# Kernel optimization log

Hardware: AMD Instinct MI355X
Metric: run time of the kernel (lower is better)

The kernel has to match this reference:

```python
import jax, jax.numpy as jnp
import numpy as np

NEG = -1000.0  # fill value for unmatched (type_mask != ti) entries

B, N, R = 4, 48, 16
T = 2 * R + 1          # 33 transition channels
Nc, L = 80, 3          # chains, chain length
Nt, Ni = 16, 5         # triples, chains per triple (uniform c_sections)


def setup_inputs() -> dict:
    key = jax.random.key(0)
    k1, k2, k3, k4, k5 = jax.random.split(key, 5)
    transitions = jax.random.normal(k1, (B, N, N, T), dtype=jnp.float32)
    type_mask = jax.random.randint(k2, (B, N, N, R), 0, 2, dtype=jnp.int32)
    rules = jax.random.randint(k3, (Nc, L), 0, T, dtype=jnp.int32)
    # stacked per-triple weights [Nt, Ni] (orig: ParameterList of [Ni,1]) and biases [Nt]
    weights = jax.random.normal(k4, (Nt, Ni), dtype=jnp.float32) / np.sqrt(Ni)
    biases = jax.random.uniform(k5, (Nt,), dtype=jnp.float32, minval=-1.0, maxval=1.0)
    return {"transitions": transitions, "type_mask": type_mask, "rules": rules,
            "weights": weights, "biases": biases}


def path_scores(transitions, rules):
    """Tropical (max-plus) chain DP.
    transitions: [B,N,N,T], rules: [Nc,L] -> scores [B,N,N,Nc]
    scores[b,x,y,c] = max over intermediate nodes of sum of hop scores.
    """
    Lc = rules.shape[1]
    hops = [transitions[..., rules[:, l]] for l in range(Lc)]  # each [B,N,N,Nc]
    # max-plus "matmul": s[b,x,y,c] = max_k hops0[b,x,k,c] + hops1[b,k,y,c]
    s = jnp.max(hops[0][:, :, :, None, :] + hops[1][:, None, :, :, :], axis=2)
    for l in range(2, Lc):
        s = jnp.max(s[:, :, :, None, :] + hops[l][:, None, :, :, :], axis=2)
    return s


def reference(transitions, type_mask, rules, weights, biases):
    # scores over all chains, exponentiated: [B,N,N,Nc]
    s = jnp.exp(path_scores(transitions, rules))
    # group chains by triple (uniform sections): [B,N,N,Nt,Ni]
    s = s.reshape(s.shape[0], s.shape[1], s.shape[2], Nt, Ni)
    # per-triple weighted sum + bias; one triple per relation so Nt == R
    comb = jnp.einsum('bxytc,tc->bxyt', s, weights) + biases  # [B,N,N,R]
    # masked_scatter: write score where type_mask[...,i] == ti (== 0 here), else -1000
    out = jnp.where(type_mask == 0, comb, NEG)
    return out
```

## Files before the change

kernel.cpp:

```cpp
#include <hip/hip_runtime.h>
#include <cmath>

#define BB 4
#define NN 48
#define NP 49
#define TT 33
#define RR 16
#define NC 80
#define NI 5

__global__ __launch_bounds__(192) void chain_dp_kernel(
    const float* __restrict__ trans,
    const int*   __restrict__ rules,
    const float* __restrict__ weights,
    float*       __restrict__ sw)
{
    __shared__ float H0T[NN * NP];
    __shared__ float H1 [NN * NN];
    __shared__ float H2 [NN * NN];
    __shared__ float S1T[NN * NP];

    const int bc = blockIdx.x;
    const int b  = bc / NC;
    const int c  = bc - b * NC;

    const int r0 = rules[c * 3 + 0];
    const int r1 = rules[c * 3 + 1];
    const int r2 = rules[c * 3 + 2];
    const float w = weights[c];

    const float* tb = trans + (size_t)b * NN * NN * TT;

    for (int i = threadIdx.x; i < NN * NN; i += 192) {
        const int x = i / NN;
        const int k = i - x * NN;
        const size_t base = (size_t)i * TT;
        H0T[k * NP + x] = tb[base + r0];
        H1[i]           = tb[base + r1];
        H2[i]           = tb[base + r2];
    }
    __syncthreads();

    const int tx = threadIdx.x & 15;
    const int ty = threadIdx.x >> 4;
    const int x0 = tx * 3;
    const int y0 = ty * 4;

    float acc[3][4];
    #pragma unroll
    for (int jx = 0; jx < 3; ++jx)
        #pragma unroll
        for (int jy = 0; jy < 4; ++jy) acc[jx][jy] = -INFINITY;

    #pragma unroll 4
    for (int k = 0; k < NN; ++k) {
        const float a0 = H0T[k * NP + x0 + 0];
        const float a1 = H0T[k * NP + x0 + 1];
        const float a2 = H0T[k * NP + x0 + 2];
        const float4 bv = *(const float4*)&H1[k * NN + y0];
        acc[0][0] = fmaxf(acc[0][0], a0 + bv.x);
        acc[0][1] = fmaxf(acc[0][1], a0 + bv.y);
        acc[0][2] = fmaxf(acc[0][2], a0 + bv.z);
        acc[0][3] = fmaxf(acc[0][3], a0 + bv.w);
        acc[1][0] = fmaxf(acc[1][0], a1 + bv.x);
        acc[1][1] = fmaxf(acc[1][1], a1 + bv.y);
        acc[1][2] = fmaxf(acc[1][2], a1 + bv.z);
        acc[1][3] = fmaxf(acc[1][3], a1 + bv.w);
        acc[2][0] = fmaxf(acc[2][0], a2 + bv.x);
        acc[2][1] = fmaxf(acc[2][1], a2 + bv.y);
        acc[2][2] = fmaxf(acc[2][2], a2 + bv.z);
        acc[2][3] = fmaxf(acc[2][3], a2 + bv.w);
    }

    #pragma unroll
    for (int jx = 0; jx < 3; ++jx)
        #pragma unroll
        for (int jy = 0; jy < 4; ++jy)
            S1T[(y0 + jy) * NP + x0 + jx] = acc[jx][jy];
    __syncthreads();

    float acc2[3][4];
    #pragma unroll
    for (int jx = 0; jx < 3; ++jx)
        #pragma unroll
        for (int jy = 0; jy < 4; ++jy) acc2[jx][jy] = -INFINITY;

    #pragma unroll 4
    for (int k = 0; k < NN; ++k) {
        const float a0 = S1T[k * NP + x0 + 0];
        const float a1 = S1T[k * NP + x0 + 1];
        const float a2 = S1T[k * NP + x0 + 2];
        const float4 bv = *(const float4*)&H2[k * NN + y0];
        acc2[0][0] = fmaxf(acc2[0][0], a0 + bv.x);
        acc2[0][1] = fmaxf(acc2[0][1], a0 + bv.y);
        acc2[0][2] = fmaxf(acc2[0][2], a0 + bv.z);
        acc2[0][3] = fmaxf(acc2[0][3], a0 + bv.w);
        acc2[1][0] = fmaxf(acc2[1][0], a1 + bv.x);
        acc2[1][1] = fmaxf(acc2[1][1], a1 + bv.y);
        acc2[1][2] = fmaxf(acc2[1][2], a1 + bv.z);
        acc2[1][3] = fmaxf(acc2[1][3], a1 + bv.w);
        acc2[2][0] = fmaxf(acc2[2][0], a2 + bv.x);
        acc2[2][1] = fmaxf(acc2[2][1], a2 + bv.y);
        acc2[2][2] = fmaxf(acc2[2][2], a2 + bv.z);
        acc2[2][3] = fmaxf(acc2[2][3], a2 + bv.w);
    }

    float* outp = sw + (size_t)bc * NN * NN;
    #pragma unroll
    for (int jx = 0; jx < 3; ++jx)
        #pragma unroll
        for (int jy = 0; jy < 4; ++jy)
            outp[(x0 + jx) * NN + y0 + jy] = __expf(acc2[jx][jy]) * w;
}

__global__ __launch_bounds__(256) void combine_kernel(
    const float* __restrict__ sw,
    const int*   __restrict__ mask,
    const float* __restrict__ biases,
    float*       __restrict__ out)
{
    const int idx = blockIdx.x * 256 + threadIdx.x;
    if (idx >= BB * NN * NN) return;
    const int b = idx / (NN * NN);
    const int p = idx - b * (NN * NN);

    const float* base = sw + (size_t)b * NC * NN * NN + p;

    float acc[RR];
    #pragma unroll
    for (int t = 0; t < RR; ++t) {
        float s = biases[t];
        #pragma unroll
        for (int i = 0; i < NI; ++i)
            s += base[(size_t)(t * NI + i) * NN * NN];
        acc[t] = s;
    }

    const int4* m4 = (const int4*)(mask + (size_t)idx * RR);
    float4*     o4 = (float4*)(out + (size_t)idx * RR);
    #pragma unroll
    for (int q = 0; q < 4; ++q) {
        const int4 m = m4[q];
        float4 o;
        o.x = (m.x == 0) ? acc[q * 4 + 0] : -1000.0f;
        o.y = (m.y == 0) ? acc[q * 4 + 1] : -1000.0f;
        o.z = (m.z == 0) ? acc[q * 4 + 2] : -1000.0f;
        o.w = (m.w == 0) ? acc[q * 4 + 3] : -1000.0f;
        o4[q] = o;
    }
}

extern "C" void kernel_launch(void* const* d_in, const int* in_sizes, int n_in,
                              void* d_out, int out_size, void* d_ws, size_t ws_size,
                              hipStream_t stream)
{
    const float* trans   = (const float*)d_in[0];
    const int*   mask    = (const int*)  d_in[1];
    const int*   rules   = (const int*)  d_in[2];
    const float* weights = (const float*)d_in[3];
    const float* biases  = (const float*)d_in[4];
    float* out = (float*)d_out;
    float* sw  = (float*)d_ws;

    chain_dp_kernel<<<BB * NC, 192, 0, stream>>>(trans, rules, weights, sw);

    const int total = BB * NN * NN;
    combine_kernel<<<(total + 255) / 256, 256, 0, stream>>>(sw, mask, biases, out);
}
```

Before: 75.47 us.

## Split chain DP over x-halves and k-halves, widen combine parallelism

The chain DP grid is doubled so that each block handles half of the x rows. Within a block the two thread groups each take half of the k reduction, and their partial maxima are merged through shared memory, which gives more blocks to fill the GPU. The combine kernel likewise splits the 16 relations across two threads per pixel. The cost is that every block still loads the full H1 and H2 matrices, so redundant global loads roughly double, and extra syncs and merge passes are added.

```diff
diff --git a/kernel.cpp b/kernel.cpp
--- a/kernel.cpp
+++ b/kernel.cpp
@@ -3,48 +3,61 @@
 
 #define BB 4
 #define NN 48
-#define NP 49
 #define TT 33
 #define RR 16
 #define NC 80
 #define NI 5
-
-__global__ __launch_bounds__(192) void chain_dp_kernel(
+#define NEG (-1000.0f)
+
+#define XS 24
+#define XP 25
+#define NTH 192
+#define NTILE 96
+
+__global__ __launch_bounds__(NTH) void chain_dp_kernel(
     const float* __restrict__ trans,
     const int*   __restrict__ rules,
     const float* __restrict__ weights,
     float*       __restrict__ sw)
 {
-    __shared__ float H0T[NN * NP];
+    __shared__ float H0T[NN * XP];
     __shared__ float H1 [NN * NN];
     __shared__ float H2 [NN * NN];
-    __shared__ float S1T[NN * NP];
-
-    const int bc = blockIdx.x;
-    const int b  = bc / NC;
-    const int c  = bc - b * NC;
+    __shared__ float S1T[NN * XP];
+    __shared__ float Pa [NN * XP];
+
+    const int blk = blockIdx.x;
+    const int bc  = blk >> 1;
+    const int xh  = blk & 1;
+    const int b   = bc / NC;
+    const int c   = bc - b * NC;
+    const int xbase = xh * XS;
 
     const int r0 = rules[c * 3 + 0];
     const int r1 = rules[c * 3 + 1];
     const int r2 = rules[c * 3 + 2];
-    const float w = weights[c];
 
     const float* tb = trans + (size_t)b * NN * NN * TT;
 
-    for (int i = threadIdx.x; i < NN * NN; i += 192) {
-        const int x = i / NN;
-        const int k = i - x * NN;
+    for (int i = threadIdx.x; i < XS * NN; i += NTH) {
+        const int xl = i / NN;
+        const int k  = i - xl * NN;
+        H0T[k * XP + xl] = tb[(size_t)((xbase + xl) * NN + k) * TT + r0];
+    }
+    for (int i = threadIdx.x; i < NN * NN; i += NTH) {
         const size_t base = (size_t)i * TT;
-        H0T[k * NP + x] = tb[base + r0];
-        H1[i]           = tb[base + r1];
-        H2[i]           = tb[base + r2];
-    }
-    __syncthreads();
-
-    const int tx = threadIdx.x & 15;
-    const int ty = threadIdx.x >> 4;
+        H1[i] = tb[base + r1];
+        H2[i] = tb[base + r2];
+    }
+    __syncthreads();
+
+    const int g  = threadIdx.x / NTILE;
+    const int w  = threadIdx.x - g * NTILE;
+    const int tx = w & 7;
+    const int ty = w >> 3;
     const int x0 = tx * 3;
     const int y0 = ty * 4;
+    const int k0 = g * 24;
 
     float acc[3][4];
     #pragma unroll
@@ -53,64 +66,87 @@
         for (int jy = 0; jy < 4; ++jy) acc[jx][jy] = -INFINITY;
 
     #pragma unroll 4
-    for (int k = 0; k < NN; ++k) {
-        const float a0 = H0T[k * NP + x0 + 0];
-        const float a1 = H0T[k * NP + x0 + 1];
-        const float a2 = H0T[k * NP + x0 + 2];
-        const float4 bv = *(const float4*)&H1[k * NN + y0];
-        acc[0][0] = fmaxf(acc[0][0], a0 + bv.x);
-        acc[0][1] = fmaxf(acc[0][1], a0 + bv.y);
-        acc[0][2] = fmaxf(acc[0][2], a0 + bv.z);
-        acc[0][3] = fmaxf(acc[0][3], a0 + bv.w);
-        acc[1][0] = fmaxf(acc[1][0], a1 + bv.x);
-        acc[1][1] = fmaxf(acc[1][1], a1 + bv.y);
-        acc[1][2] = fmaxf(acc[1][2], a1 + bv.z);
-        acc[1][3] = fmaxf(acc[1][3], a1 + bv.w);
-        acc[2][0] = fmaxf(acc[2][0], a2 + bv.x);
-        acc[2][1] = fmaxf(acc[2][1], a2 + bv.y);
-        acc[2][2] = fmaxf(acc[2][2], a2 + bv.z);
-        acc[2][3] = fmaxf(acc[2][3], a2 + bv.w);
-    }
-
+    for (int kp = 0; kp < 12; ++kp) {
+        const int k = k0 + kp * 2;
+        float a0[3], a1[3];
+        #pragma unroll
+        for (int jx = 0; jx < 3; ++jx) {
+            a0[jx] = H0T[k * XP + x0 + jx];
+            a1[jx] = H0T[(k + 1) * XP + x0 + jx];
+        }
+        const float4 bv0 = *(const float4*)&H1[k * NN + y0];
+        const float4 bv1 = *(const float4*)&H1[(k + 1) * NN + y0];
+        const float b0[4] = {bv0.x, bv0.y, bv0.z, bv0.w};
+        const float b1[4] = {bv1.x, bv1.y, bv1.z, bv1.w};
+        #pragma unroll
+        for (int jx = 0; jx < 3; ++jx)
+            #pragma unroll
+            for (int jy = 0; jy < 4; ++jy)
+                acc[jx][jy] = fmaxf(acc[jx][jy],
+                                    fmaxf(a0[jx] + b0[jy], a1[jx] + b1[jy]));
+    }
+
+    {
+        float* dst = (g == 0) ? S1T : Pa;
+        #pragma unroll
+        for (int jx = 0; jx < 3; ++jx)
+            #pragma unroll
+            for (int jy = 0; jy < 4; ++jy)
+                dst[(y0 + jy) * XP + x0 + jx] = acc[jx][jy];
+    }
+    __syncthreads();
+
+    for (int j = threadIdx.x; j < NN * XP; j += NTH)
+        S1T[j] = fmaxf(S1T[j], Pa[j]);
+    __syncthreads();
+
+    float acc2[3][4];
     #pragma unroll
     for (int jx = 0; jx < 3; ++jx)
         #pragma unroll
-        for (int jy = 0; jy < 4; ++jy)
-            S1T[(y0 + jy) * NP + x0 + jx] = acc[jx][jy];
-    __syncthreads();
-
-    float acc2[3][4];
-    #pragma unroll
-    for (int jx = 0; jx < 3; ++jx)
-        #pragma unroll
         for (int jy = 0; jy < 4; ++jy) acc2[jx][jy] = -INFINITY;
 
     #pragma unroll 4
-    for (int k = 0; k < NN; ++k) {
-        const float a0 = S1T[k * NP + x0 + 0];
-        const float a1 = S1T[k * NP + x0 + 1];
-        const float a2 = S1T[k * NP + x0 + 2];
-        const float4 bv = *(const float4*)&H2[k * NN + y0];
-        acc2[0][0] = fmaxf(acc2[0][0], a0 + bv.x);
-        acc2[0][1] = fmaxf(acc2[0][1], a0 + bv.y);
-        acc2[0][2] = fmaxf(acc2[0][2], a0 + bv.z);
-        acc2[0][3] = fmaxf(acc2[0][3], a0 + bv.w);
-        acc2[1][0] = fmaxf(acc2[1][0], a1 + bv.x);
-        acc2[1][1] = fmaxf(acc2[1][1], a1 + bv.y);
-        acc2[1][2] = fmaxf(acc2[1][2], a1 + bv.z);
-        acc2[1][3] = fmaxf(acc2[1][3], a1 + bv.w);
-        acc2[2][0] = fmaxf(acc2[2][0], a2 + bv.x);
-        acc2[2][1] = fmaxf(acc2[2][1], a2 + bv.y);
-        acc2[2][2] = fmaxf(acc2[2][2], a2 + bv.z);
-        acc2[2][3] = fmaxf(acc2[2][3], a2 + bv.w);
-    }
-
-    float* outp = sw + (size_t)bc * NN * NN;
-    #pragma unroll
-    for (int jx = 0; jx < 3; ++jx)
-        #pragma unroll
-        for (int jy = 0; jy < 4; ++jy)
-            outp[(x0 + jx) * NN + y0 + jy] = __expf(acc2[jx][jy]) * w;
+    for (int kp = 0; kp < 12; ++kp) {
+        const int k = k0 + kp * 2;
+        float a0[3], a1[3];
+        #pragma unroll
+        for (int jx = 0; jx < 3; ++jx) {
+            a0[jx] = S1T[k * XP + x0 + jx];
+            a1[jx] = S1T[(k + 1) * XP + x0 + jx];
+        }
+        const float4 bv0 = *(const float4*)&H2[k * NN + y0];
+        const float4 bv1 = *(const float4*)&H2[(k + 1) * NN + y0];
+        const float b0[4] = {bv0.x, bv0.y, bv0.z, bv0.w};
+        const float b1[4] = {bv1.x, bv1.y, bv1.z, bv1.w};
+        #pragma unroll
+        for (int jx = 0; jx < 3; ++jx)
+            #pragma unroll
+            for (int jy = 0; jy < 4; ++jy)
+                acc2[jx][jy] = fmaxf(acc2[jx][jy],
+                                     fmaxf(a0[jx] + b0[jy], a1[jx] + b1[jy]));
+    }
+
+    if (g == 1) {
+        #pragma unroll
+        for (int jx = 0; jx < 3; ++jx)
+            #pragma unroll
+            for (int jy = 0; jy < 4; ++jy)
+                Pa[(jx * 4 + jy) * NTILE + w] = acc2[jx][jy];
+    }
+    __syncthreads();
+
+    if (g == 0) {
+        const float wgt = weights[c];
+        float* outp = sw + (size_t)bc * NN * NN;
+        #pragma unroll
+        for (int jx = 0; jx < 3; ++jx)
+            #pragma unroll
+            for (int jy = 0; jy < 4; ++jy) {
+                const float m = fmaxf(acc2[jx][jy], Pa[(jx * 4 + jy) * NTILE + w]);
+                outp[(xbase + x0 + jx) * NN + y0 + jy] = __expf(m) * wgt;
+            }
+    }
 }
 
 __global__ __launch_bounds__(256) void combine_kernel(
@@ -119,33 +155,35 @@
     const float* __restrict__ biases,
     float*       __restrict__ out)
 {
-    const int idx = blockIdx.x * 256 + threadIdx.x;
-    if (idx >= BB * NN * NN) return;
-    const int b = idx / (NN * NN);
-    const int p = idx - b * (NN * NN);
+    const int tq = threadIdx.x >> 7;
+    const int pl = blockIdx.x * 128 + (threadIdx.x & 127);
+    if (pl >= BB * NN * NN) return;
+    const int b = pl / (NN * NN);
+    const int p = pl - b * (NN * NN);
 
     const float* base = sw + (size_t)b * NC * NN * NN + p;
 
-    float acc[RR];
-    #pragma unroll
-    for (int t = 0; t < RR; ++t) {
+    float acc[8];
+    #pragma unroll
+    for (int tt = 0; tt < 8; ++tt) {
+        const int t = tq * 8 + tt;
         float s = biases[t];
         #pragma unroll
         for (int i = 0; i < NI; ++i)
             s += base[(size_t)(t * NI + i) * NN * NN];
-        acc[t] = s;
-    }
-
-    const int4* m4 = (const int4*)(mask + (size_t)idx * RR);
-    float4*     o4 = (float4*)(out + (size_t)idx * RR);
-    #pragma unroll
-    for (int q = 0; q < 4; ++q) {
+        acc[tt] = s;
+    }
+
+    const int4* m4 = (const int4*)(mask + (size_t)pl * RR + tq * 8);
+    float4*     o4 = (float4*)(out + (size_t)pl * RR + tq * 8);
+    #pragma unroll
+    for (int q = 0; q < 2; ++q) {
         const int4 m = m4[q];
         float4 o;
-        o.x = (m.x == 0) ? acc[q * 4 + 0] : -1000.0f;
-        o.y = (m.y == 0) ? acc[q * 4 + 1] : -1000.0f;
-        o.z = (m.z == 0) ? acc[q * 4 + 2] : -1000.0f;
-        o.w = (m.w == 0) ? acc[q * 4 + 3] : -1000.0f;
+        o.x = (m.x == 0) ? acc[q * 4 + 0] : NEG;
+        o.y = (m.y == 0) ? acc[q * 4 + 1] : NEG;
+        o.z = (m.z == 0) ? acc[q * 4 + 2] : NEG;
+        o.w = (m.w == 0) ? acc[q * 4 + 3] : NEG;
         o4[q] = o;
     }
 }
@@ -162,8 +200,8 @@
     float* out = (float*)d_out;
     float* sw  = (float*)d_ws;
 
-    chain_dp_kernel<<<BB * NC, 192, 0, stream>>>(trans, rules, weights, sw);
-
-    const int total = BB * NN * NN;
-    combine_kernel<<<(total + 255) / 256, 256, 0, stream>>>(sw, mask, biases, out);
+    chain_dp_kernel<<<BB * NC * 2, NTH, 0, stream>>>(trans, rules, weights, sw);
+
+    const int total2 = BB * NN * NN * 2;
+    combine_kernel<<<(total2 + 255) / 256, 256, 0, stream>>>(sw, mask, biases, out);
 }
```

Result: slower. 78.99 us (+4.7%).
